# Kernel tuning notes

Hardware: AMD Instinct MI355X
Metric: run time of the kernel (lower is better)

## Reference

```python
import jax, jax.numpy as jnp
import numpy as np

N = 8192       # nodes
IN_F = 512     # in_features
OUT_F = 256    # out_features


def setup_inputs() -> dict:
    key = jax.random.key(0)
    k1, k2, k3, k4 = jax.random.split(key, 4)
    # xavier_uniform-like scales for params
    w_scale = 1.414 * (6.0 / (IN_F + OUT_F)) ** 0.5
    a_scale = 1.414 * (6.0 / (2 * OUT_F + 1)) ** 0.5
    x = jax.random.normal(k1, (N, IN_F), jnp.float32)
    W = jax.random.uniform(k2, (IN_F, OUT_F), jnp.float32, -w_scale, w_scale)
    a = jax.random.uniform(k3, (2 * OUT_F, 1), jnp.float32, -a_scale, a_scale)
    adj = jax.random.randint(k4, (N, N), 0, 2, jnp.int32)
    return {"x": x, "W": W, "a": a, "adj": adj}


def reference(x, W, a, adj):
    # h = x @ W : [N, OUT_F]
    h = x @ W
    f = W.shape[1]
    a1, a2 = a[:f], a[f:]          # each [OUT_F, 1]
    # Original builds a_input[i,j] = concat(h_i, h_j) then matmuls with a.
    # Equivalent decomposition: e[i,j] = h_i . a1 + h_j . a2
    e = (h @ a1) + (h @ a2).T      # [N, N]
    neg = jnp.float32(-9e15)
    attention = jnp.where(adj > 0, e, neg)   # no softmax in the original
    h_prime = attention @ h        # [N, OUT_F]
    return h_prime
```

## Files before the change

### kernel.cpp

```cpp
#include <hip/hip_runtime.h>


#define NEG_BIG (-9000000000000000.0f)

typedef __bf16 bf16x8 __attribute__((ext_vector_type(8)));
typedef float f32x16 __attribute__((ext_vector_type(16)));

static __device__ __forceinline__ unsigned short f2bf(float f) {
  unsigned u = __builtin_bit_cast(unsigned, f);
  u = u + 0x7FFFu + ((u >> 16) & 1u);
  return (unsigned short)(u >> 16);
}
static __device__ __forceinline__ float bfbits2f(unsigned hi16) {
  return __builtin_bit_cast(float, hi16 << 16);
}
static __device__ __forceinline__ unsigned pk2(float a, float b) {
  return (unsigned)f2bf(a) | ((unsigned)f2bf(b) << 16);
}
static __device__ __forceinline__ bf16x8 asbf(int4 q) {
  return __builtin_bit_cast(bf16x8, q);
}
static __device__ __forceinline__ f32x16 mfma(bf16x8 a, int4 b, f32x16 c) {
  return __builtin_amdgcn_mfma_f32_32x32x16_bf16(a, asbf(b), c, 0, 0, 0);
}
static __device__ __forceinline__ unsigned bp(unsigned da, unsigned db, int p) {
  return (((da >> p) & 1u) | (((db >> p) & 1u) << 16)) * 0x3F80u;
}
static __device__ __forceinline__ bf16x8 mkfrag(unsigned dA, unsigned dB,
                                                unsigned dC, unsigned dD, int p0) {
  uint4 u;
  u.x = bp(dA, dB, p0);
  u.y = bp(dC, dD, p0);
  u.z = bp(dA, dB, p0 + 1);
  u.w = bp(dC, dD, p0 + 1);
  return __builtin_bit_cast(bf16x8, u);
}

__global__ __launch_bounds__(256) void k0_bits(const int* __restrict__ adj,
    unsigned long long* __restrict__ bm) {
  const int w = threadIdx.x >> 6, l = threadIdx.x & 63;
  const int row = blockIdx.x * 4 + w;
  const int4* ar = (const int4*)(adj + (size_t)row * 8192) + l;
  unsigned long long* br = bm + (size_t)row * 128;
#pragma unroll 2
  for (int b = 0; b < 32; ++b) {
    int4 v = ar[b * 64];
    unsigned long long b0 = __ballot(v.x > 0);
    unsigned long long b1 = __ballot(v.y > 0);
    unsigned long long b2 = __ballot(v.z > 0);
    unsigned long long b3 = __ballot(v.w > 0);
    if (l == 0) {
      ulonglong2* p = (ulonglong2*)(br + (size_t)b * 4);
      p[0] = make_ulonglong2(b0, b1);
      p[1] = make_ulonglong2(b2, b3);
    }
  }
}

__global__ void k1a_wt(const float* __restrict__ W, unsigned short* __restrict__ WT,
                       float* __restrict__ T) {
  const int i = blockIdx.x * 256 + threadIdx.x;
  const int k = i >> 8, n = i & 255;
  WT[n * 512 + k] = f2bf(W[i]);
  if (blockIdx.x == 0) T[threadIdx.x] = 0.f;
}

__global__ __launch_bounds__(256) void k1b_h(const float* __restrict__ x,
    const unsigned short* __restrict__ WT, unsigned short* __restrict__ hP) {
  __shared__ unsigned short XS[64 * 264];
  const int t = threadIdx.x;
  const int mt = blockIdx.x;
  const int m0 = mt << 5;
  const int row = t >> 3, c7 = t & 7;
  const float* xr = x + (size_t)(m0 + row) * 512 + c7 * 4;
  const int gb = c7 >> 1, off = (t & 1) * 4;
#pragma unroll
  for (int j = 0; j < 16; ++j) {
    float4 v = *(const float4*)(xr + 32 * j);
    *(uint2*)&XS[(gb + 4 * j) * 264 + row * 8 + off] =
        make_uint2(pk2(v.x, v.y), pk2(v.z, v.w));
  }
  __syncthreads();
  const int w = t >> 6, l = t & 63, l31 = l & 31, lh = l >> 5;
  f32x16 acc0, acc1;
  for (int i = 0; i < 16; ++i) { acc0[i] = 0.f; acc1[i] = 0.f; }
  const int nt0 = w * 2;
  const unsigned short* w0 = WT + (size_t)(nt0 * 32 + l31) * 512 + lh * 8;
  const unsigned short* w1 = w0 + 32 * 512;
  const char* XB = (const char*)XS + lh * 528 + l31 * 16;
#pragma unroll 4
  for (int ks = 0; ks < 32; ++ks) {
    bf16x8 Af = *(const bf16x8*)(XB + ks * 1056);
    int4 b0 = *(const int4*)(w0 + ks * 16);
    int4 b1 = *(const int4*)(w1 + ks * 16);
    acc0 = mfma(Af, b0, acc0);
    acc1 = mfma(Af, b1, acc1);
  }
#pragma unroll
  for (int reg = 0; reg < 16; ++reg) {
    const int mm = (reg & 3) + 8 * (reg >> 2) + 4 * lh;
    hP[(size_t)mt * 8192 + (nt0 * 32 + l31) * 32 + mm] = f2bf(acc0[reg]);
    hP[(size_t)mt * 8192 + ((nt0 + 1) * 32 + l31) * 32 + mm] = f2bf(acc1[reg]);
  }
}

__global__ __launch_bounds__(256) void k2_colsum(const unsigned short* __restrict__ hP,
                                                 float* __restrict__ T) {
  const int t = threadIdx.x;
  const int b = blockIdx.x;
  const int4* p = (const int4*)(hP + (size_t)b * 8192 + t * 32);
  int4 q0 = p[0], q1 = p[1], q2 = p[2], q3 = p[3];
  float s = 0.f;
  const unsigned* u0 = (const unsigned*)&q0;
  const unsigned* u1 = (const unsigned*)&q1;
  const unsigned* u2 = (const unsigned*)&q2;
  const unsigned* u3 = (const unsigned*)&q3;
#pragma unroll
  for (int i = 0; i < 4; ++i) {
    s += bfbits2f(u0[i] & 0xFFFFu) + bfbits2f(u0[i] >> 16);
    s += bfbits2f(u1[i] & 0xFFFFu) + bfbits2f(u1[i] >> 16);
    s += bfbits2f(u2[i] & 0xFFFFu) + bfbits2f(u2[i] >> 16);
    s += bfbits2f(u3[i] & 0xFFFFu) + bfbits2f(u3[i] >> 16);
  }
  atomicAdd(&T[t], s);
}

__global__ __launch_bounds__(256, 1) void k3_att(
    const unsigned long long* __restrict__ bm,
    const unsigned short* __restrict__ hP, const float* __restrict__ T,
    float* __restrict__ out) {
  __shared__ float red[2][64][64];
  const int t = threadIdx.x, blk = blockIdx.x;
  const int w = t >> 6, l = t & 63, l31 = l & 31, lh = l >> 5;
  const int ch = w & 1, s = w >> 1;
  const int rb = blk >> 1, cb = blk & 1;
  const int r0 = rb * 64;
  const int cw0 = cb * 128 + ch * 64;
  const int lh2 = lh * 2;

  const int4* bmp0 = (const int4*)bm + (size_t)(r0 + l31) * 64 + s * 32;
  const int4* bmp1 = bmp0 + 32 * 64;
  const unsigned short* hB = hP + (size_t)(cw0 + l31) * 32 + lh * 8;

  f32x16 acc[2][2];
#pragma unroll
  for (int mt = 0; mt < 2; ++mt)
#pragma unroll
    for (int nt = 0; nt < 2; ++nt)
#pragma unroll
      for (int i = 0; i < 16; ++i) acc[mt][nt][i] = 0.f;

  int4 qA0[2], qA1[2], qB0[2], qB1[2], BvA[4], BvB[4];
  int jt = s * 128;

#define LOADBM(k, Q0, Q1)                                                   \
  Q0[0] = bmp0[(k) * 2]; Q0[1] = bmp0[(k) * 2 + 1];                         \
  Q1[0] = bmp1[(k) * 2]; Q1[1] = bmp1[(k) * 2 + 1];

#define ITER(mm, Q0, Q1, BVC, BVN)                                          \
  {                                                                         \
    {                                                                       \
      const unsigned short* hb_ = hB + (size_t)(jt + 1) * 8192;             \
      BVN[0] = *(const int4*)(hb_);                                         \
      BVN[1] = *(const int4*)(hb_ + 16);                                    \
      BVN[2] = *(const int4*)(hb_ + 1024);                                  \
      BVN[3] = *(const int4*)(hb_ + 1040);                                  \
    }                                                                       \
    const unsigned* q0_ = (const unsigned*)(Q0);                            \
    const unsigned* q1_ = (const unsigned*)(Q1);                            \
    const unsigned a0_ = q0_[((mm) >> 2)];                                  \
    const unsigned b0_ = q0_[2 + ((mm) >> 2)];                              \
    const unsigned c0_ = q0_[4 + ((mm) >> 2)];                              \
    const unsigned d0_ = q0_[6 + ((mm) >> 2)];                              \
    const unsigned a1_ = q1_[((mm) >> 2)];                                  \
    const unsigned b1_ = q1_[2 + ((mm) >> 2)];                              \
    const unsigned c1_ = q1_[4 + ((mm) >> 2)];                              \
    const unsigned d1_ = q1_[6 + ((mm) >> 2)];                              \
    const int pb_ = 8 * ((mm) & 3) + lh2;                                   \
    bf16x8 A00 = mkfrag(a0_, b0_, c0_, d0_, pb_);              \
    bf16x8 A01 = mkfrag(a0_, b0_, c0_, d0_, pb_ + 4);          \
    bf16x8 A10 = mkfrag(a1_, b1_, c1_, d1_, pb_);              \
    bf16x8 A11 = mkfrag(a1_, b1_, c1_, d1_, pb_ + 4);          \
    acc[0][0] = mfma(A00, BVC[0], acc[0][0]);                               \
    acc[1][0] = mfma(A10, BVC[0], acc[1][0]);                               \
    acc[0][1] = mfma(A00, BVC[2], acc[0][1]);                               \
    acc[1][1] = mfma(A10, BVC[2], acc[1][1]);                               \
    acc[0][0] = mfma(A01, BVC[1], acc[0][0]);                               \
    acc[1][0] = mfma(A11, BVC[1], acc[1][0]);                               \
    acc[0][1] = mfma(A01, BVC[3], acc[0][1]);                               \
    acc[1][1] = mfma(A11, BVC[3], acc[1][1]);                               \
    ++jt;                                                                   \
  }

  LOADBM(0, qA0, qA1)
  {
    const unsigned short* hb_ = hB + (size_t)jt * 8192;
    BvA[0] = *(const int4*)(hb_);
    BvA[1] = *(const int4*)(hb_ + 16);
    BvA[2] = *(const int4*)(hb_ + 1024);
    BvA[3] = *(const int4*)(hb_ + 1040);
  }

#pragma unroll 1
  for (int bb = 0; bb < 8; ++bb) {
    LOADBM(bb * 2 + 1, qB0, qB1)
    ITER(0, qA0, qA1, BvA, BvB)
    ITER(1, qA0, qA1, BvB, BvA)
    ITER(2, qA0, qA1, BvA, BvB)
    ITER(3, qA0, qA1, BvB, BvA)
    ITER(4, qA0, qA1, BvA, BvB)
    ITER(5, qA0, qA1, BvB, BvA)
    ITER(6, qA0, qA1, BvA, BvB)
    ITER(7, qA0, qA1, BvB, BvA)
    LOADBM(bb * 2 + 2, qA0, qA1)
    ITER(0, qB0, qB1, BvA, BvB)
    ITER(1, qB0, qB1, BvB, BvA)
    ITER(2, qB0, qB1, BvA, BvB)
    ITER(3, qB0, qB1, BvB, BvA)
    ITER(4, qB0, qB1, BvA, BvB)
    ITER(5, qB0, qB1, BvB, BvA)
    ITER(6, qB0, qB1, BvA, BvB)
    ITER(7, qB0, qB1, BvB, BvA)
  }
#undef ITER
#undef LOADBM

  if (s == 1) {
#pragma unroll
    for (int mt = 0; mt < 2; ++mt)
#pragma unroll
      for (int nt = 0; nt < 2; ++nt)
#pragma unroll
        for (int reg = 0; reg < 16; ++reg)
          red[ch][(mt * 2 + nt) * 16 + reg][l] = acc[mt][nt][reg];
  }
  __syncthreads();
  if (s == 0) {
#pragma unroll
    for (int mt = 0; mt < 2; ++mt)
#pragma unroll
      for (int nt = 0; nt < 2; ++nt) {
        const int cc = cw0 + nt * 32 + l31;
        const float tv = T[cc];
#pragma unroll
        for (int reg = 0; reg < 16; ++reg) {
          const float am = acc[mt][nt][reg] + red[ch][(mt * 2 + nt) * 16 + reg][l];
          const int rr = r0 + mt * 32 + (reg & 3) + 8 * (reg >> 2) + 4 * lh;
          out[(size_t)rr * 256 + cc] = NEG_BIG * (tv - am);
        }
      }
  }
}

extern "C" void kernel_launch(void* const* d_in, const int* in_sizes, int n_in,
                              void* d_out, int out_size, void* d_ws, size_t ws_size,
                              hipStream_t stream) {
  const float* x = (const float*)d_in[0];
  const float* W = (const float*)d_in[1];
  const int* adj = (const int*)d_in[3];
  float* out = (float*)d_out;
  char* ws = (char*)d_ws;
  unsigned short* WT = (unsigned short*)(ws);
  unsigned short* hP = (unsigned short*)(ws + (1 << 20));
  float* T = (float*)(ws + (6 << 20));
  unsigned long long* bm = (unsigned long long*)(ws + (8 << 20));

  k0_bits<<<2048, 256, 0, stream>>>(adj, bm);
  k1a_wt<<<512, 256, 0, stream>>>(W, WT, T);
  k1b_h<<<256, 256, 0, stream>>>(x, WT, hP);
  k2_colsum<<<256, 256, 0, stream>>>(hP, T);
  k3_att<<<256, 256, 0, stream>>>(bm, hP, T, out);
}
```

Before: 442.0 us.

## Split attention K-loop four ways and simplify bitmask-to-bf16 fragment expansion

Reorders the K-dimension inside each 32-row group of the h layout so that each lane's bf16 fragment maps to contiguous bits of one byte of the adjacency bitmask. The per-fragment bit expansion becomes byte extraction plus shift-and-mask, replacing the per-bit extraction done before. The attention kernel also changes how work is divided. Each block now covers 64 columns with four waves splitting K four ways, instead of two column halves by two K halves. The grid doubles to 512 blocks, and launch bounds are raised to 2 blocks per CU for more parallelism. The costs are a larger LDS reduction buffer, a three-way reduction, and more register pressure under the occupancy hint.

```diff
diff --git a/kernel.cpp b/kernel.cpp
--- a/kernel.cpp
+++ b/kernel.cpp
@@ -22,18 +22,6 @@
 }
 static __device__ __forceinline__ f32x16 mfma(bf16x8 a, int4 b, f32x16 c) {
   return __builtin_amdgcn_mfma_f32_32x32x16_bf16(a, asbf(b), c, 0, 0, 0);
-}
-static __device__ __forceinline__ unsigned bp(unsigned da, unsigned db, int p) {
-  return (((da >> p) & 1u) | (((db >> p) & 1u) << 16)) * 0x3F80u;
-}
-static __device__ __forceinline__ bf16x8 mkfrag(unsigned dA, unsigned dB,
-                                                unsigned dC, unsigned dD, int p0) {
-  uint4 u;
-  u.x = bp(dA, dB, p0);
-  u.y = bp(dC, dD, p0);
-  u.z = bp(dA, dB, p0 + 1);
-  u.w = bp(dC, dD, p0 + 1);
-  return __builtin_bit_cast(bf16x8, u);
 }
 
 __global__ __launch_bounds__(256) void k0_bits(const int* __restrict__ adj,
@@ -99,8 +87,9 @@
 #pragma unroll
   for (int reg = 0; reg < 16; ++reg) {
     const int mm = (reg & 3) + 8 * (reg >> 2) + 4 * lh;
-    hP[(size_t)mt * 8192 + (nt0 * 32 + l31) * 32 + mm] = f2bf(acc0[reg]);
-    hP[(size_t)mt * 8192 + ((nt0 + 1) * 32 + l31) * 32 + mm] = f2bf(acc1[reg]);
+    const int sl = ((mm >> 1) & 1) * 16 + (mm & 1) * 8 + (mm >> 2);
+    hP[(size_t)mt * 8192 + (nt0 * 32 + l31) * 32 + sl] = f2bf(acc0[reg]);
+    hP[(size_t)mt * 8192 + ((nt0 + 1) * 32 + l31) * 32 + sl] = f2bf(acc1[reg]);
   }
 }
 
@@ -125,21 +114,20 @@
   atomicAdd(&T[t], s);
 }
 
-__global__ __launch_bounds__(256, 1) void k3_att(
+__global__ __launch_bounds__(256, 2) void k3_att(
     const unsigned long long* __restrict__ bm,
     const unsigned short* __restrict__ hP, const float* __restrict__ T,
     float* __restrict__ out) {
-  __shared__ float red[2][64][64];
+  __shared__ float red[3][64][64];
   const int t = threadIdx.x, blk = blockIdx.x;
   const int w = t >> 6, l = t & 63, l31 = l & 31, lh = l >> 5;
-  const int ch = w & 1, s = w >> 1;
-  const int rb = blk >> 1, cb = blk & 1;
+  const int s = w;
+  const int rb = blk >> 2, cb = blk & 3;
   const int r0 = rb * 64;
-  const int cw0 = cb * 128 + ch * 64;
-  const int lh2 = lh * 2;
-
-  const int4* bmp0 = (const int4*)bm + (size_t)(r0 + l31) * 64 + s * 32;
-  const int4* bmp1 = bmp0 + 32 * 64;
+  const int cw0 = cb * 64;
+
+  const char* bmr0 = (const char*)bm + (size_t)(r0 + l31) * 1024 + s * 256 + lh * 8;
+  const char* bmr1 = bmr0 + 32 * 1024;
   const unsigned short* hB = hP + (size_t)(cw0 + l31) * 32 + lh * 8;
 
   f32x16 acc[2][2];
@@ -150,14 +138,27 @@
 #pragma unroll
       for (int i = 0; i < 16; ++i) acc[mt][nt][i] = 0.f;
 
-  int4 qA0[2], qA1[2], qB0[2], qB1[2], BvA[4], BvB[4];
-  int jt = s * 128;
-
-#define LOADBM(k, Q0, Q1)                                                   \
-  Q0[0] = bmp0[(k) * 2]; Q0[1] = bmp0[(k) * 2 + 1];                         \
-  Q1[0] = bmp1[(k) * 2]; Q1[1] = bmp1[(k) * 2 + 1];
-
-#define ITER(mm, Q0, Q1, BVC, BVN)                                          \
+  uint2 pA0a, pA0b, pA1a, pA1b, pB0a, pB0b, pB1a, pB1b;
+  int4 BvA[4], BvB[4];
+  int jt = s * 64;
+
+#define LOADBM(k, A0a, A0b, A1a, A1b)                                       \
+  A0a = *(const uint2*)(bmr0 + (k) * 32);                                   \
+  A0b = *(const uint2*)(bmr0 + (k) * 32 + 16);                              \
+  A1a = *(const uint2*)(bmr1 + (k) * 32);                                   \
+  A1b = *(const uint2*)(bmr1 + (k) * 32 + 16);
+
+#define XP(dw, m3, u4)                                                      \
+  {                                                                         \
+    const unsigned bb_ = ((dw) >> (8 * (m3))) & 0xFFu;                      \
+    const unsigned tt_ = bb_ | (bb_ << 15);                                 \
+    u4.x = ((tt_)&0x00010001u) * 0x3F80u;                                   \
+    u4.y = ((tt_ >> 2) & 0x00010001u) * 0x3F80u;                            \
+    u4.z = ((tt_ >> 4) & 0x00010001u) * 0x3F80u;                            \
+    u4.w = ((tt_ >> 6) & 0x00010001u) * 0x3F80u;                            \
+  }
+
+#define ITER(mm, A0a, A0b, A1a, A1b, BVC, BVN)                              \
   {                                                                         \
     {                                                                       \
       const unsigned short* hb_ = hB + (size_t)(jt + 1) * 8192;             \
@@ -166,33 +167,31 @@
       BVN[2] = *(const int4*)(hb_ + 1024);                                  \
       BVN[3] = *(const int4*)(hb_ + 1040);                                  \
     }                                                                       \
-    const unsigned* q0_ = (const unsigned*)(Q0);                            \
-    const unsigned* q1_ = (const unsigned*)(Q1);                            \
-    const unsigned a0_ = q0_[((mm) >> 2)];                                  \
-    const unsigned b0_ = q0_[2 + ((mm) >> 2)];                              \
-    const unsigned c0_ = q0_[4 + ((mm) >> 2)];                              \
-    const unsigned d0_ = q0_[6 + ((mm) >> 2)];                              \
-    const unsigned a1_ = q1_[((mm) >> 2)];                                  \
-    const unsigned b1_ = q1_[2 + ((mm) >> 2)];                              \
-    const unsigned c1_ = q1_[4 + ((mm) >> 2)];                              \
-    const unsigned d1_ = q1_[6 + ((mm) >> 2)];                              \
-    const int pb_ = 8 * ((mm) & 3) + lh2;                                   \
-    bf16x8 A00 = mkfrag(a0_, b0_, c0_, d0_, pb_);              \
-    bf16x8 A01 = mkfrag(a0_, b0_, c0_, d0_, pb_ + 4);          \
-    bf16x8 A10 = mkfrag(a1_, b1_, c1_, d1_, pb_);              \
-    bf16x8 A11 = mkfrag(a1_, b1_, c1_, d1_, pb_ + 4);          \
-    acc[0][0] = mfma(A00, BVC[0], acc[0][0]);                               \
-    acc[1][0] = mfma(A10, BVC[0], acc[1][0]);                               \
-    acc[0][1] = mfma(A00, BVC[2], acc[0][1]);                               \
-    acc[1][1] = mfma(A10, BVC[2], acc[1][1]);                               \
-    acc[0][0] = mfma(A01, BVC[1], acc[0][0]);                               \
-    acc[1][0] = mfma(A11, BVC[1], acc[1][0]);                               \
-    acc[0][1] = mfma(A01, BVC[3], acc[0][1]);                               \
-    acc[1][1] = mfma(A11, BVC[3], acc[1][1]);                               \
+    const unsigned d00_ = ((mm) >> 2) ? A0a.y : A0a.x;         \
+    const unsigned d01_ = ((mm) >> 2) ? A0b.y : A0b.x;         \
+    const unsigned d10_ = ((mm) >> 2) ? A1a.y : A1a.x;         \
+    const unsigned d11_ = ((mm) >> 2) ? A1b.y : A1b.x;         \
+    uint4 u00_, u01_, u10_, u11_;                                           \
+    XP(d00_, (mm)&3, u00_)                                                  \
+    XP(d01_, (mm)&3, u01_)                                                  \
+    XP(d10_, (mm)&3, u10_)                                                  \
+    XP(d11_, (mm)&3, u11_)                                                  \
+    const bf16x8 A00_ = __builtin_bit_cast(bf16x8, u00_);                   \
+    const bf16x8 A01_ = __builtin_bit_cast(bf16x8, u01_);                   \
+    const bf16x8 A10_ = __builtin_bit_cast(bf16x8, u10_);                   \
+    const bf16x8 A11_ = __builtin_bit_cast(bf16x8, u11_);                   \
+    acc[0][0] = mfma(A00_, BVC[0], acc[0][0]);                              \
+    acc[1][0] = mfma(A10_, BVC[0], acc[1][0]);                              \
+    acc[0][1] = mfma(A00_, BVC[2], acc[0][1]);                              \
+    acc[1][1] = mfma(A10_, BVC[2], acc[1][1]);                              \
+    acc[0][0] = mfma(A01_, BVC[1], acc[0][0]);                              \
+    acc[1][0] = mfma(A11_, BVC[1], acc[1][0]);                              \
+    acc[0][1] = mfma(A01_, BVC[3], acc[0][1]);                              \
+    acc[1][1] = mfma(A11_, BVC[3], acc[1][1]);                              \
     ++jt;                                                                   \
   }
 
-  LOADBM(0, qA0, qA1)
+  LOADBM(0, pA0a, pA0b, pA1a, pA1b)
   {
     const unsigned short* hb_ = hB + (size_t)jt * 8192;
     BvA[0] = *(const int4*)(hb_);
@@ -202,37 +201,38 @@
   }
 
 #pragma unroll 1
-  for (int bb = 0; bb < 8; ++bb) {
-    LOADBM(bb * 2 + 1, qB0, qB1)
-    ITER(0, qA0, qA1, BvA, BvB)
-    ITER(1, qA0, qA1, BvB, BvA)
-    ITER(2, qA0, qA1, BvA, BvB)
-    ITER(3, qA0, qA1, BvB, BvA)
-    ITER(4, qA0, qA1, BvA, BvB)
-    ITER(5, qA0, qA1, BvB, BvA)
-    ITER(6, qA0, qA1, BvA, BvB)
-    ITER(7, qA0, qA1, BvB, BvA)
-    LOADBM(bb * 2 + 2, qA0, qA1)
-    ITER(0, qB0, qB1, BvA, BvB)
-    ITER(1, qB0, qB1, BvB, BvA)
-    ITER(2, qB0, qB1, BvA, BvB)
-    ITER(3, qB0, qB1, BvB, BvA)
-    ITER(4, qB0, qB1, BvA, BvB)
-    ITER(5, qB0, qB1, BvB, BvA)
-    ITER(6, qB0, qB1, BvA, BvB)
-    ITER(7, qB0, qB1, BvB, BvA)
+  for (int b2 = 0; b2 < 8; b2 += 2) {
+    LOADBM(b2 + 1, pB0a, pB0b, pB1a, pB1b)
+    ITER(0, pA0a, pA0b, pA1a, pA1b, BvA, BvB)
+    ITER(1, pA0a, pA0b, pA1a, pA1b, BvB, BvA)
+    ITER(2, pA0a, pA0b, pA1a, pA1b, BvA, BvB)
+    ITER(3, pA0a, pA0b, pA1a, pA1b, BvB, BvA)
+    ITER(4, pA0a, pA0b, pA1a, pA1b, BvA, BvB)
+    ITER(5, pA0a, pA0b, pA1a, pA1b, BvB, BvA)
+    ITER(6, pA0a, pA0b, pA1a, pA1b, BvA, BvB)
+    ITER(7, pA0a, pA0b, pA1a, pA1b, BvB, BvA)
+    if (b2 + 2 < 8) { LOADBM(b2 + 2, pA0a, pA0b, pA1a, pA1b) }
+    ITER(0, pB0a, pB0b, pB1a, pB1b, BvA, BvB)
+    ITER(1, pB0a, pB0b, pB1a, pB1b, BvB, BvA)
+    ITER(2, pB0a, pB0b, pB1a, pB1b, BvA, BvB)
+    ITER(3, pB0a, pB0b, pB1a, pB1b, BvB, BvA)
+    ITER(4, pB0a, pB0b, pB1a, pB1b, BvA, BvB)
+    ITER(5, pB0a, pB0b, pB1a, pB1b, BvB, BvA)
+    ITER(6, pB0a, pB0b, pB1a, pB1b, BvA, BvB)
+    ITER(7, pB0a, pB0b, pB1a, pB1b, BvB, BvA)
   }
 #undef ITER
+#undef XP
 #undef LOADBM
 
-  if (s == 1) {
+  if (s > 0) {
 #pragma unroll
     for (int mt = 0; mt < 2; ++mt)
 #pragma unroll
       for (int nt = 0; nt < 2; ++nt)
 #pragma unroll
         for (int reg = 0; reg < 16; ++reg)
-          red[ch][(mt * 2 + nt) * 16 + reg][l] = acc[mt][nt][reg];
+          red[s - 1][(mt * 2 + nt) * 16 + reg][l] = acc[mt][nt][reg];
   }
   __syncthreads();
   if (s == 0) {
@@ -244,7 +244,9 @@
         const float tv = T[cc];
 #pragma unroll
         for (int reg = 0; reg < 16; ++reg) {
-          const float am = acc[mt][nt][reg] + red[ch][(mt * 2 + nt) * 16 + reg][l];
+          const int idx = (mt * 2 + nt) * 16 + reg;
+          const float am = acc[mt][nt][reg] + red[0][idx][l] +
+                           red[1][idx][l] + red[2][idx][l];
           const int rr = r0 + mt * 32 + (reg & 3) + 8 * (reg >> 2) + 4 * lh;
           out[(size_t)rr * 256 + cc] = NEG_BIG * (tv - am);
         }
@@ -269,5 +271,5 @@
   k1a_wt<<<512, 256, 0, stream>>>(W, WT, T);
   k1b_h<<<256, 256, 0, stream>>>(x, WT, hP);
   k2_colsum<<<256, 256, 0, stream>>>(hP, T);
-  k3_att<<<256, 256, 0, stream>>>(bm, hP, T, out);
-}
+  k3_att<<<512, 256, 0, stream>>>(bm, hP, T, out);
+}
```

Result: no change. 441.3 us (-0.2%).
